# Optimization experiments

Measured on AMD Instinct MI355X. Metric: run time of the kernel, lower is better.

## Reference

```python
import jax, jax.numpy as jnp
import numpy as np

HEAD_NUM = 8
NEG = 10000.0


def setup_inputs() -> dict:
    key = jax.random.key(0)
    ks = jax.random.split(key, 8)
    B, S, D = 2, 2048, 512
    sc = 1.0 / np.sqrt(D)
    return {
        "x": jax.random.normal(ks[0], (B, S, D), dtype=jnp.float32),
        "mask": jax.random.randint(ks[1], (B, S), 0, 2, dtype=jnp.int32),
        "Wq": jax.random.normal(ks[2], (D, D), dtype=jnp.float32) * sc,
        "bq": jnp.zeros((D,), jnp.float32),
        "Wk": jax.random.normal(ks[3], (D, D), dtype=jnp.float32) * sc,
        "bk": jnp.zeros((D,), jnp.float32),
        "Wv": jax.random.normal(ks[4], (D, D), dtype=jnp.float32) * sc,
        "bv": jnp.zeros((D,), jnp.float32),
        "Wo": jax.random.normal(ks[5], (D, D), dtype=jnp.float32) * sc,
        "bo": jnp.zeros((D,), jnp.float32),
    }


def _split_heads(t, H):
    B, S, D = t.shape
    return t.reshape(B, S, H, D // H).transpose(0, 2, 1, 3)  # [B,H,S,hd]


def reference(x, mask, Wq, bq, Wk, bk, Wv, bv, Wo, bo):
    B, S, D = x.shape
    H = HEAD_NUM
    hd = D // H
    # linear projections + relu activation (as in keras layer)
    q = jax.nn.relu(x @ Wq + bq)
    k = jax.nn.relu(x @ Wk + bk)
    v = jax.nn.relu(x @ Wv + bv)
    q = _split_heads(q, H)
    k = _split_heads(k, H)
    v = _split_heads(v, H)
    # scaled dot-product scores: scale by sqrt(head_dim) (query last dim after split)
    e = jnp.einsum("bhqd,bhkd->bhqk", q, k) / jnp.sqrt(jnp.float32(hd))
    # causal (history_only) additive mask
    idx = jnp.arange(S)
    causal = (idx[None, :] > idx[:, None]).astype(jnp.float32)  # [S,S]
    e = e - NEG * causal[None, None, :, :]
    # key padding mask, additive
    e = e - NEG * (1.0 - mask.astype(jnp.float32))[:, None, None, :]
    # stable softmax (explicit max-subtract as in source)
    a = jax.nn.softmax(e, axis=-1)
    out = jnp.einsum("bhqk,bhkd->bhqd", a, v)  # [B,H,S,hd]
    out = out.transpose(0, 2, 1, 3).reshape(B, S, D)
    # output projection + activation
    return jax.nn.relu(out @ Wo + bo)
```

## Files before the change

### kernel.cpp

```cpp
#include <hip/hip_runtime.h>
#include <hip/hip_bf16.h>

constexpr int Bc = 2, Sc = 2048, Dc = 512, Hc = 8, HDc = 64;
constexpr int Mtot = Bc * Sc;
constexpr size_t HEADMAT = (size_t)Bc * Hc * Sc * HDc;
constexpr float SC2  = 0.18033688011112042f;
constexpr float NEG2 = 14426.950408889634f;

typedef __attribute__((ext_vector_type(8))) short          short8;
typedef __attribute__((ext_vector_type(8))) unsigned short ushort8;
typedef __attribute__((ext_vector_type(4))) float          f32x4;

#define MFMA16 __builtin_amdgcn_mfma_f32_16x16x32_bf16

static __device__ __forceinline__ unsigned short f32_to_bf16_bits(float f) {
    unsigned int u = __builtin_bit_cast(unsigned int, f);
    unsigned int r = u + 0x7FFFu + ((u >> 16) & 1u);
    return (unsigned short)(r >> 16);
}

__global__ __launch_bounds__(256)
void convert_x(const float* __restrict__ x, unsigned short* __restrict__ Xb, int n)
{
    const int i = (blockIdx.x * 256 + threadIdx.x) * 4;
    if (i >= n) return;
    const float4 v = *(const float4*)(x + i);
    ushort4 o;
    o.x = f32_to_bf16_bits(v.x);
    o.y = f32_to_bf16_bits(v.y);
    o.z = f32_to_bf16_bits(v.z);
    o.w = f32_to_bf16_bits(v.w);
    *(ushort4*)(Xb + i) = o;
}

__global__ __launch_bounds__(256)
void transpose_w(const float* __restrict__ W0, const float* __restrict__ W1,
                 const float* __restrict__ W2, const float* __restrict__ W3,
                 unsigned short* __restrict__ Wt)
{
    __shared__ float T[64][65];
    const int z = blockIdx.z;
    const float* Wp = (z == 0) ? W0 : (z == 1) ? W1 : (z == 2) ? W2 : W3;
    unsigned short* Op = Wt + (size_t)z * 512 * 512;

    const int kt = blockIdx.y * 64, nt = blockIdx.x * 64;
    const int t = threadIdx.x;
    const int r  = t >> 2, c4 = (t & 3) * 16;

    #pragma unroll
    for (int i = 0; i < 4; ++i) {
        const float4 v = *(const float4*)(Wp + (size_t)(kt + r) * 512 + nt + c4 + 4 * i);
        T[r][c4 + 4*i + 0] = v.x;
        T[r][c4 + 4*i + 1] = v.y;
        T[r][c4 + 4*i + 2] = v.z;
        T[r][c4 + 4*i + 3] = v.w;
    }
    __syncthreads();

    const int n = t >> 2, k4 = (t & 3) * 16;
    #pragma unroll
    for (int i = 0; i < 4; ++i) {
        ushort4 o;
        o.x = f32_to_bf16_bits(T[k4 + 4*i + 0][n]);
        o.y = f32_to_bf16_bits(T[k4 + 4*i + 1][n]);
        o.z = f32_to_bf16_bits(T[k4 + 4*i + 2][n]);
        o.w = f32_to_bf16_bits(T[k4 + 4*i + 3][n]);
        *(ushort4*)(Op + (size_t)(nt + n) * 512 + kt + k4 + 4 * i) = o;
    }
}

template<bool HEADOUT>
__global__ __launch_bounds__(256)
void gemm_tile(const unsigned short* __restrict__ Xb,
               const unsigned short* __restrict__ Wt,
               const float* __restrict__ b0, const float* __restrict__ b1,
               const float* __restrict__ b2,
               unsigned short* __restrict__ Hout,
               float* __restrict__ Yf)
{
    __shared__ short As[128 * 32];
    __shared__ short Bs[64 * 32];

    const int lane = threadIdx.x & 63, wave = threadIdx.x >> 6;
    const int c = lane & 15, g = lane >> 4;
    const int wr = wave >> 1, wc = wave & 1;
    const int z = blockIdx.z;
    const unsigned short* Wp = Wt + (size_t)z * 512 * 512;
    const float* bp = (z == 0) ? b0 : (z == 1) ? b1 : b2;
    const int bm = blockIdx.y * 128;
    const int bn = blockIdx.x * 64;

    const int srow = lane >> 2;
    const int scol = (lane & 3) * 8;

    f32x4 acc[4][2] = {};

    for (int k0 = 0; k0 < 512; k0 += 32) {
        __syncthreads();
        #pragma unroll
        for (int i = 0; i < 2; ++i) {
            const int row = (wave * 2 + i) * 16 + srow;
            const short8 v = *(const short8*)(Xb + (size_t)(bm + row) * 512 + k0 + scol);
            *(short8*)(&As[row * 32 + scol]) = v;
        }
        {
            const int row = wave * 16 + srow;
            const short8 v = *(const short8*)(Wp + (size_t)(bn + row) * 512 + k0 + scol);
            *(short8*)(&Bs[row * 32 + scol]) = v;
        }
        __syncthreads();

        short8 a[4], bfr[2];
        #pragma unroll
        for (int mi = 0; mi < 4; ++mi)
            a[mi] = *(const short8*)(&As[(wr * 64 + mi * 16 + c) * 32 + g * 8]);
        #pragma unroll
        for (int ni = 0; ni < 2; ++ni)
            bfr[ni] = *(const short8*)(&Bs[(wc * 32 + ni * 16 + c) * 32 + g * 8]);
        #pragma unroll
        for (int mi = 0; mi < 4; ++mi)
            #pragma unroll
            for (int ni = 0; ni < 2; ++ni)
                acc[mi][ni] = MFMA16(a[mi], bfr[ni], acc[mi][ni], 0, 0, 0);
    }

    #pragma unroll
    for (int mi = 0; mi < 4; ++mi) {
        #pragma unroll
        for (int ni = 0; ni < 2; ++ni) {
            const int n = bn + wc * 32 + ni * 16 + c;
            const float bias = bp[n];
            float v[4];
            #pragma unroll
            for (int r = 0; r < 4; ++r)
                v[r] = fmaxf(acc[mi][ni][r] + bias, 0.0f);
            const int mbase = bm + wr * 64 + mi * 16 + 4 * g;
            if constexpr (HEADOUT) {
                const int bb = mbase >> 11, ss = mbase & 2047;
                const int hh = n >> 6, hd = n & 63;
                #pragma unroll
                for (int r = 0; r < 4; ++r)
                    Hout[(size_t)z * HEADMAT +
                         (((size_t)(bb * Hc + hh) * Sc + ss + r) * HDc + hd)] =
                        f32_to_bf16_bits(v[r]);
            } else {
                #pragma unroll
                for (int r = 0; r < 4; ++r)
                    Yf[(size_t)(mbase + r) * 512 + n] = v[r];
            }
        }
    }
}

__global__ __launch_bounds__(256)
void attn_mfma(const short* __restrict__ Qh, const short* __restrict__ Kh,
               const short* __restrict__ Vh, const int* __restrict__ mask,
               unsigned short* __restrict__ Ob)
{
    __shared__ __align__(16) char smem[4 * 9216];

    const int lane = threadIdx.x & 63;
    const int wave = threadIdx.x >> 6;
    const int bid  = blockIdx.x;
    const int swz  = (bid & 7) * 128 + (bid >> 3);
    const int qt   = swz & 63;
    const int h    = (swz >> 6) & 7;
    const int b    = swz >> 9;
    const int q0   = qt * 32;
    const int c    = lane & 15;
    const int g    = lane >> 4;

    char*  wbase = smem + wave * 9216;
    short* vst   = (short*)wbase;
    float* Lacc  = (float*)wbase;
    float* Lml   = (float*)(wbase + 8704);

    const size_t headoff = (size_t)(b * Hc + h) * Sc * HDc;
    const short* Qp = Qh + headoff;
    const short* Kp = Kh + headoff;
    const short* Vp = Vh + headoff;
    const int* mb = mask + b * Sc;

    int fb = Sc;
    for (int base = 0; base < Sc; base += 64) {
        unsigned long long bal = __ballot(mb[base + lane] != 0);
        if (bal) { fb = base + (__ffsll(bal) - 1); break; }
    }
    const int kmax = (fb <= q0) ? (q0 + 32) : Sc;
    const int kend = (kmax + 31) & ~31;
    const int nT   = kend >> 5;
    const int tpw  = (nT + 3) >> 2;
    const int kbeg = wave * tpw * 32;
    const int kfin = min(kend, kbeg + tpw * 32);

    const short8 qa0 = *(const short8*)(Qp + (size_t)(q0 + c) * HDc + g * 8);
    const short8 qa1 = *(const short8*)(Qp + (size_t)(q0 + c) * HDc + 32 + g * 8);
    const short8 qb0 = *(const short8*)(Qp + (size_t)(q0 + 16 + c) * HDc + g * 8);
    const short8 qb1 = *(const short8*)(Qp + (size_t)(q0 + 16 + c) * HDc + 32 + g * 8);

    f32x4 accA[4] = {{0,0,0,0},{0,0,0,0},{0,0,0,0},{0,0,0,0}};
    f32x4 accB[4] = {{0,0,0,0},{0,0,0,0},{0,0,0,0},{0,0,0,0}};
    float mA = -1e30f, lA = 0.f, mB = -1e30f, lB = 0.f;

    const int vrow = lane >> 1;
    const int vcol = (lane & 1) * 32;

    for (int k0 = kbeg; k0 < kfin; k0 += 32) {
        const short* vsrc = Vp + (size_t)(k0 + vrow) * HDc + vcol;
        const ushort8 vr0 = *(const ushort8*)(vsrc + 0);
        const ushort8 vr1 = *(const ushort8*)(vsrc + 8);
        const ushort8 vr2 = *(const ushort8*)(vsrc + 16);
        const ushort8 vr3 = *(const ushort8*)(vsrc + 24);

        const short8 kf0a = *(const short8*)(Kp + (size_t)(k0 + c) * HDc + g * 8);
        const short8 kf0b = *(const short8*)(Kp + (size_t)(k0 + c) * HDc + 32 + g * 8);
        const short8 kf1a = *(const short8*)(Kp + (size_t)(k0 + 16 + c) * HDc + g * 8);
        const short8 kf1b = *(const short8*)(Kp + (size_t)(k0 + 16 + c) * HDc + 32 + g * 8);

        f32x4 sa0 = {0,0,0,0}, sa1 = {0,0,0,0};
        f32x4 sb0 = {0,0,0,0}, sb1 = {0,0,0,0};
        sa0 = MFMA16(kf0a, qa0, sa0, 0, 0, 0);
        sa0 = MFMA16(kf0b, qa1, sa0, 0, 0, 0);
        sa1 = MFMA16(kf1a, qa0, sa1, 0, 0, 0);
        sa1 = MFMA16(kf1b, qa1, sa1, 0, 0, 0);
        sb0 = MFMA16(kf0a, qb0, sb0, 0, 0, 0);
        sb0 = MFMA16(kf0b, qb1, sb0, 0, 0, 0);
        sb1 = MFMA16(kf1a, qb0, sb1, 0, 0, 0);
        sb1 = MFMA16(kf1b, qb1, sb1, 0, 0, 0);

        const int4 mka = *(const int4*)(mb + k0 + 4 * g);
        const int4 mkb = *(const int4*)(mb + k0 + 16 + 4 * g);
        const int mia[4] = {mka.x, mka.y, mka.z, mka.w};
        const int mib[4] = {mkb.x, mkb.y, mkb.z, mkb.w};

        float eA[8], eB[8];
        float tA = -1e30f, tB = -1e30f;
        if (k0 + 31 > q0) {
            #pragma unroll
            for (int r = 0; r < 4; ++r) {
                const int ka = k0 + 4 * g + r;
                const int kb = k0 + 16 + 4 * g + r;
                float e0 = sa0[r] * SC2; if (ka > q0 + c)      e0 -= NEG2;
                float e1 = sa1[r] * SC2; if (kb > q0 + c)      e1 -= NEG2;
                float e2 = sb0[r] * SC2; if (ka > q0 + 16 + c) e2 -= NEG2;
                float e3 = sb1[r] * SC2; if (kb > q0 + 16 + c) e3 -= NEG2;
                if (mia[r] == 0) { e0 -= NEG2; e2 -= NEG2; }
                if (mib[r] == 0) { e1 -= NEG2; e3 -= NEG2; }
                eA[r] = e0; eA[4 + r] = e1; tA = fmaxf(tA, fmaxf(e0, e1));
                eB[r] = e2; eB[4 + r] = e3; tB = fmaxf(tB, fmaxf(e2, e3));
            }
        } else {
            #pragma unroll
            for (int r = 0; r < 4; ++r) {
                float e0 = sa0[r] * SC2;
                float e1 = sa1[r] * SC2;
                float e2 = sb0[r] * SC2;
                float e3 = sb1[r] * SC2;
                if (mia[r] == 0) { e0 -= NEG2; e2 -= NEG2; }
                if (mib[r] == 0) { e1 -= NEG2; e3 -= NEG2; }
                eA[r] = e0; eA[4 + r] = e1; tA = fmaxf(tA, fmaxf(e0, e1));
                eB[r] = e2; eB[4 + r] = e3; tB = fmaxf(tB, fmaxf(e2, e3));
            }
        }
        tA = fmaxf(tA, __shfl_xor(tA, 16));
        tB = fmaxf(tB, __shfl_xor(tB, 16));
        tA = fmaxf(tA, __shfl_xor(tA, 32));
        tB = fmaxf(tB, __shfl_xor(tB, 32));

        if (__any(tA > mA)) {
            const float mn = fmaxf(mA, tA);
            const float corr = __builtin_exp2f(mA - mn);
            mA = mn; lA *= corr;
            float cq[4];
            #pragma unroll
            for (int r = 0; r < 4; ++r) cq[r] = __shfl(corr, 4 * g + r);
            #pragma unroll
            for (int t = 0; t < 4; ++t)
                #pragma unroll
                for (int r = 0; r < 4; ++r) accA[t][r] *= cq[r];
        }
        if (__any(tB > mB)) {
            const float mn = fmaxf(mB, tB);
            const float corr = __builtin_exp2f(mB - mn);
            mB = mn; lB *= corr;
            float cq[4];
            #pragma unroll
            for (int r = 0; r < 4; ++r) cq[r] = __shfl(corr, 4 * g + r);
            #pragma unroll
            for (int t = 0; t < 4; ++t)
                #pragma unroll
                for (int r = 0; r < 4; ++r) accB[t][r] *= cq[r];
        }

        float pA[8], pB[8], psA = 0.f, psB = 0.f;
        #pragma unroll
        for (int j = 0; j < 8; ++j) {
            pA[j] = __builtin_exp2f(eA[j] - mA); psA += pA[j];
            pB[j] = __builtin_exp2f(eB[j] - mB); psB += pB[j];
        }
        lA += psA; lB += psB;

        short8 pfa, pfb;
        #pragma unroll
        for (int j = 0; j < 8; ++j) {
            pfa[j] = (short)f32_to_bf16_bits(pA[j]);
            pfb[j] = (short)f32_to_bf16_bits(pB[j]);
        }

        short* vdst = vst + vrow * 72 + vcol;
        *(ushort8*)(vdst + 0)  = vr0;
        *(ushort8*)(vdst + 8)  = vr1;
        *(ushort8*)(vdst + 16) = vr2;
        *(ushort8*)(vdst + 24) = vr3;

        #pragma unroll
        for (int t = 0; t < 4; ++t) {
            short8 vf;
            #pragma unroll
            for (int j = 0; j < 4; ++j) {
                vf[j]     = vst[(4 * g + j) * 72      + t * 16 + c];
                vf[4 + j] = vst[(16 + 4 * g + j) * 72 + t * 16 + c];
            }
            accA[t] = MFMA16(pfa, vf, accA[t], 0, 0, 0);
            accB[t] = MFMA16(pfb, vf, accB[t], 0, 0, 0);
        }
    }

    lA += __shfl_xor(lA, 16); lA += __shfl_xor(lA, 32);
    lB += __shfl_xor(lB, 16); lB += __shfl_xor(lB, 32);

    if (g == 0) {
        Lml[c]      = mA;  Lml[16 + c] = mB;
        Lml[32 + c] = lA;  Lml[48 + c] = lB;
    }
    #pragma unroll
    for (int t = 0; t < 4; ++t)
        #pragma unroll
        for (int r = 0; r < 4; ++r) {
            Lacc[(4 * g + r) * 68 + t * 16 + c]      = accA[t][r];
            Lacc[(16 + 4 * g + r) * 68 + t * 16 + c] = accB[t][r];
        }
    __syncthreads();

    const int col = wave * 16 + c;
    #pragma unroll
    for (int half = 0; half < 2; ++half)
        #pragma unroll
        for (int r = 0; r < 4; ++r) {
            const int row = half * 16 + 4 * g + r;
            float mu[4], lu[4], ou[4], M = -1e30f;
            #pragma unroll
            for (int u = 0; u < 4; ++u) {
                const float* LaccU = (const float*)(smem + u * 9216);
                const float* LmlU  = (const float*)(smem + u * 9216 + 8704);
                mu[u] = LmlU[row];
                lu[u] = LmlU[32 + row];
                ou[u] = LaccU[row * 68 + col];
                M = fmaxf(M, mu[u]);
            }
            float L = 0.f, o = 0.f;
            #pragma unroll
            for (int u = 0; u < 4; ++u) {
                const float w = __builtin_exp2f(mu[u] - M);
                L += w * lu[u];
                o += w * ou[u];
            }
            Ob[(size_t)(b * Sc + q0 + row) * Dc + h * HDc + col] =
                f32_to_bf16_bits(o / L);
        }
}

extern "C" void kernel_launch(void* const* d_in, const int* in_sizes, int n_in,
                              void* d_out, int out_size, void* d_ws, size_t ws_size,
                              hipStream_t stream) {
    const float* x  = (const float*)d_in[0];
    const int* mask = (const int*)d_in[1];
    const float* Wq = (const float*)d_in[2];
    const float* bq = (const float*)d_in[3];
    const float* Wk = (const float*)d_in[4];
    const float* bk = (const float*)d_in[5];
    const float* Wv = (const float*)d_in[6];
    const float* bv = (const float*)d_in[7];
    const float* Wo = (const float*)d_in[8];
    const float* bo = (const float*)d_in[9];
    float* out = (float*)d_out;

    unsigned short* Xb = (unsigned short*)d_ws;
    unsigned short* Wt = Xb + (size_t)Mtot * 512;
    unsigned short* Qh = Wt + (size_t)4 * 512 * 512;
    unsigned short* Kh = Qh + HEADMAT;
    unsigned short* Vh = Kh + HEADMAT;
    unsigned short* Ob = Vh + HEADMAT;

    convert_x<<<dim3((Mtot * 512) / 1024), dim3(256), 0, stream>>>(
        x, Xb, Mtot * 512);
    transpose_w<<<dim3(8, 8, 4), dim3(256), 0, stream>>>(Wq, Wk, Wv, Wo, Wt);
    gemm_tile<true><<<dim3(8, Mtot / 128, 3), dim3(256), 0, stream>>>(
        Xb, Wt, bq, bk, bv, Qh, nullptr);
    attn_mfma<<<dim3(1024), dim3(256), 0, stream>>>(
        (const short*)Qh, (const short*)Kh, (const short*)Vh, mask, Ob);
    gemm_tile<false><<<dim3(8, Mtot / 128, 1), dim3(256), 0, stream>>>(
        Ob, Wt + (size_t)3 * 512 * 512, bo, bo, bo, nullptr, out);
}
```

Before: 109.7 us.

## Pair early and late 16-row query tiles per block to balance causal work

Each block now handles two 16-row query tiles, one near the start and one near the end of the sequence (p and 127-p), instead of one contiguous 32-row tile. When causal truncation applies, this balances per-block key-loop work across the grid. In exchange the K and V tiles are no longer shared between the two query halves, so each block loads K/V twice over its key ranges and issues half as many MFMAs per K load.

```diff
diff --git a/kernel.cpp b/kernel.cpp
--- a/kernel.cpp
+++ b/kernel.cpp
@@ -163,10 +163,11 @@
     const int wave = threadIdx.x >> 6;
     const int bid  = blockIdx.x;
     const int swz  = (bid & 7) * 128 + (bid >> 3);
-    const int qt   = swz & 63;
+    const int p    = swz & 63;
     const int h    = (swz >> 6) & 7;
     const int b    = swz >> 9;
-    const int q0   = qt * 32;
+    const int q0A  = p * 16;
+    const int q0B  = (127 - p) * 16;
     const int c    = lane & 15;
     const int g    = lane >> 4;
 
@@ -186,145 +187,118 @@
         unsigned long long bal = __ballot(mb[base + lane] != 0);
         if (bal) { fb = base + (__ffsll(bal) - 1); break; }
     }
-    const int kmax = (fb <= q0) ? (q0 + 32) : Sc;
-    const int kend = (kmax + 31) & ~31;
-    const int nT   = kend >> 5;
-    const int tpw  = (nT + 3) >> 2;
-    const int kbeg = wave * tpw * 32;
-    const int kfin = min(kend, kbeg + tpw * 32);
-
-    const short8 qa0 = *(const short8*)(Qp + (size_t)(q0 + c) * HDc + g * 8);
-    const short8 qa1 = *(const short8*)(Qp + (size_t)(q0 + c) * HDc + 32 + g * 8);
-    const short8 qb0 = *(const short8*)(Qp + (size_t)(q0 + 16 + c) * HDc + g * 8);
-    const short8 qb1 = *(const short8*)(Qp + (size_t)(q0 + 16 + c) * HDc + 32 + g * 8);
+
+    const int vrow = lane >> 1;
+    const int vcol = (lane & 1) * 32;
 
     f32x4 accA[4] = {{0,0,0,0},{0,0,0,0},{0,0,0,0},{0,0,0,0}};
     f32x4 accB[4] = {{0,0,0,0},{0,0,0,0},{0,0,0,0},{0,0,0,0}};
     float mA = -1e30f, lA = 0.f, mB = -1e30f, lB = 0.f;
 
-    const int vrow = lane >> 1;
-    const int vcol = (lane & 1) * 32;
-
-    for (int k0 = kbeg; k0 < kfin; k0 += 32) {
-        const short* vsrc = Vp + (size_t)(k0 + vrow) * HDc + vcol;
-        const ushort8 vr0 = *(const ushort8*)(vsrc + 0);
-        const ushort8 vr1 = *(const ushort8*)(vsrc + 8);
-        const ushort8 vr2 = *(const ushort8*)(vsrc + 16);
-        const ushort8 vr3 = *(const ushort8*)(vsrc + 24);
-
-        const short8 kf0a = *(const short8*)(Kp + (size_t)(k0 + c) * HDc + g * 8);
-        const short8 kf0b = *(const short8*)(Kp + (size_t)(k0 + c) * HDc + 32 + g * 8);
-        const short8 kf1a = *(const short8*)(Kp + (size_t)(k0 + 16 + c) * HDc + g * 8);
-        const short8 kf1b = *(const short8*)(Kp + (size_t)(k0 + 16 + c) * HDc + 32 + g * 8);
-
-        f32x4 sa0 = {0,0,0,0}, sa1 = {0,0,0,0};
-        f32x4 sb0 = {0,0,0,0}, sb1 = {0,0,0,0};
-        sa0 = MFMA16(kf0a, qa0, sa0, 0, 0, 0);
-        sa0 = MFMA16(kf0b, qa1, sa0, 0, 0, 0);
-        sa1 = MFMA16(kf1a, qa0, sa1, 0, 0, 0);
-        sa1 = MFMA16(kf1b, qa1, sa1, 0, 0, 0);
-        sb0 = MFMA16(kf0a, qb0, sb0, 0, 0, 0);
-        sb0 = MFMA16(kf0b, qb1, sb0, 0, 0, 0);
-        sb1 = MFMA16(kf1a, qb0, sb1, 0, 0, 0);
-        sb1 = MFMA16(kf1b, qb1, sb1, 0, 0, 0);
-
-        const int4 mka = *(const int4*)(mb + k0 + 4 * g);
-        const int4 mkb = *(const int4*)(mb + k0 + 16 + 4 * g);
-        const int mia[4] = {mka.x, mka.y, mka.z, mka.w};
-        const int mib[4] = {mkb.x, mkb.y, mkb.z, mkb.w};
-
-        float eA[8], eB[8];
-        float tA = -1e30f, tB = -1e30f;
-        if (k0 + 31 > q0) {
-            #pragma unroll
-            for (int r = 0; r < 4; ++r) {
-                const int ka = k0 + 4 * g + r;
-                const int kb = k0 + 16 + 4 * g + r;
-                float e0 = sa0[r] * SC2; if (ka > q0 + c)      e0 -= NEG2;
-                float e1 = sa1[r] * SC2; if (kb > q0 + c)      e1 -= NEG2;
-                float e2 = sb0[r] * SC2; if (ka > q0 + 16 + c) e2 -= NEG2;
-                float e3 = sb1[r] * SC2; if (kb > q0 + 16 + c) e3 -= NEG2;
-                if (mia[r] == 0) { e0 -= NEG2; e2 -= NEG2; }
-                if (mib[r] == 0) { e1 -= NEG2; e3 -= NEG2; }
-                eA[r] = e0; eA[4 + r] = e1; tA = fmaxf(tA, fmaxf(e0, e1));
-                eB[r] = e2; eB[4 + r] = e3; tB = fmaxf(tB, fmaxf(e2, e3));
-            }
-        } else {
-            #pragma unroll
-            for (int r = 0; r < 4; ++r) {
-                float e0 = sa0[r] * SC2;
-                float e1 = sa1[r] * SC2;
-                float e2 = sb0[r] * SC2;
-                float e3 = sb1[r] * SC2;
-                if (mia[r] == 0) { e0 -= NEG2; e2 -= NEG2; }
-                if (mib[r] == 0) { e1 -= NEG2; e3 -= NEG2; }
-                eA[r] = e0; eA[4 + r] = e1; tA = fmaxf(tA, fmaxf(e0, e1));
-                eB[r] = e2; eB[4 + r] = e3; tB = fmaxf(tB, fmaxf(e2, e3));
-            }
-        }
-        tA = fmaxf(tA, __shfl_xor(tA, 16));
-        tB = fmaxf(tB, __shfl_xor(tB, 16));
-        tA = fmaxf(tA, __shfl_xor(tA, 32));
-        tB = fmaxf(tB, __shfl_xor(tB, 32));
-
-        if (__any(tA > mA)) {
-            const float mn = fmaxf(mA, tA);
-            const float corr = __builtin_exp2f(mA - mn);
-            mA = mn; lA *= corr;
-            float cq[4];
-            #pragma unroll
-            for (int r = 0; r < 4; ++r) cq[r] = __shfl(corr, 4 * g + r);
-            #pragma unroll
-            for (int t = 0; t < 4; ++t)
-                #pragma unroll
-                for (int r = 0; r < 4; ++r) accA[t][r] *= cq[r];
-        }
-        if (__any(tB > mB)) {
-            const float mn = fmaxf(mB, tB);
-            const float corr = __builtin_exp2f(mB - mn);
-            mB = mn; lB *= corr;
-            float cq[4];
-            #pragma unroll
-            for (int r = 0; r < 4; ++r) cq[r] = __shfl(corr, 4 * g + r);
-            #pragma unroll
-            for (int t = 0; t < 4; ++t)
-                #pragma unroll
-                for (int r = 0; r < 4; ++r) accB[t][r] *= cq[r];
-        }
-
-        float pA[8], pB[8], psA = 0.f, psB = 0.f;
-        #pragma unroll
-        for (int j = 0; j < 8; ++j) {
-            pA[j] = __builtin_exp2f(eA[j] - mA); psA += pA[j];
-            pB[j] = __builtin_exp2f(eB[j] - mB); psB += pB[j];
-        }
-        lA += psA; lB += psB;
-
-        short8 pfa, pfb;
-        #pragma unroll
-        for (int j = 0; j < 8; ++j) {
-            pfa[j] = (short)f32_to_bf16_bits(pA[j]);
-            pfb[j] = (short)f32_to_bf16_bits(pB[j]);
-        }
-
-        short* vdst = vst + vrow * 72 + vcol;
-        *(ushort8*)(vdst + 0)  = vr0;
-        *(ushort8*)(vdst + 8)  = vr1;
-        *(ushort8*)(vdst + 16) = vr2;
-        *(ushort8*)(vdst + 24) = vr3;
-
-        #pragma unroll
-        for (int t = 0; t < 4; ++t) {
-            short8 vf;
-            #pragma unroll
-            for (int j = 0; j < 4; ++j) {
-                vf[j]     = vst[(4 * g + j) * 72      + t * 16 + c];
-                vf[4 + j] = vst[(16 + 4 * g + j) * 72 + t * 16 + c];
-            }
-            accA[t] = MFMA16(pfa, vf, accA[t], 0, 0, 0);
-            accB[t] = MFMA16(pfb, vf, accB[t], 0, 0, 0);
-        }
-    }
+#define TILE_LOOP(q0X, accX, mX, lX, qx0, qx1)                                 \
+    {                                                                          \
+        const int kmax = (fb <= (q0X)) ? ((q0X) + 16) : Sc;                    \
+        const int kend = (kmax + 31) & ~31;                                    \
+        const int nT   = kend >> 5;                                            \
+        const int tpw  = (nT + 3) >> 2;                                        \
+        const int kbeg = wave * tpw * 32;                                      \
+        const int kfin = min(kend, kbeg + tpw * 32);                           \
+        for (int k0 = kbeg; k0 < kfin; k0 += 32) {                             \
+            const short* vsrc = Vp + (size_t)(k0 + vrow) * HDc + vcol;         \
+            const ushort8 vr0 = *(const ushort8*)(vsrc + 0);                   \
+            const ushort8 vr1 = *(const ushort8*)(vsrc + 8);                   \
+            const ushort8 vr2 = *(const ushort8*)(vsrc + 16);                  \
+            const ushort8 vr3 = *(const ushort8*)(vsrc + 24);                  \
+            const short8 kf0a = *(const short8*)(Kp + (size_t)(k0 + c) * HDc + g * 8);        \
+            const short8 kf0b = *(const short8*)(Kp + (size_t)(k0 + c) * HDc + 32 + g * 8);   \
+            const short8 kf1a = *(const short8*)(Kp + (size_t)(k0 + 16 + c) * HDc + g * 8);   \
+            const short8 kf1b = *(const short8*)(Kp + (size_t)(k0 + 16 + c) * HDc + 32 + g * 8);\
+            f32x4 s0 = {0,0,0,0}, s1 = {0,0,0,0};                              \
+            s0 = MFMA16(kf0a, qx0, s0, 0, 0, 0);                               \
+            s0 = MFMA16(kf0b, qx1, s0, 0, 0, 0);                               \
+            s1 = MFMA16(kf1a, qx0, s1, 0, 0, 0);                               \
+            s1 = MFMA16(kf1b, qx1, s1, 0, 0, 0);                               \
+            const int4 mka = *(const int4*)(mb + k0 + 4 * g);                  \
+            const int4 mkb = *(const int4*)(mb + k0 + 16 + 4 * g);             \
+            const int mia[4] = {mka.x, mka.y, mka.z, mka.w};                   \
+            const int mib[4] = {mkb.x, mkb.y, mkb.z, mkb.w};                   \
+            float e[8];                                                        \
+            float tmax = -1e30f;                                               \
+            if (k0 + 31 > (q0X)) {                                             \
+                _Pragma("unroll")                                              \
+                for (int r = 0; r < 4; ++r) {                                  \
+                    const int ka = k0 + 4 * g + r;                             \
+                    const int kb2 = k0 + 16 + 4 * g + r;                       \
+                    float e0 = s0[r] * SC2; if (ka  > (q0X) + c) e0 -= NEG2;   \
+                    float e1 = s1[r] * SC2; if (kb2 > (q0X) + c) e1 -= NEG2;   \
+                    if (mia[r] == 0) e0 -= NEG2;                               \
+                    if (mib[r] == 0) e1 -= NEG2;                               \
+                    e[r] = e0; e[4 + r] = e1;                                  \
+                    tmax = fmaxf(tmax, fmaxf(e0, e1));                         \
+                }                                                              \
+            } else {                                                           \
+                _Pragma("unroll")                                              \
+                for (int r = 0; r < 4; ++r) {                                  \
+                    float e0 = s0[r] * SC2;                                    \
+                    float e1 = s1[r] * SC2;                                    \
+                    if (mia[r] == 0) e0 -= NEG2;                               \
+                    if (mib[r] == 0) e1 -= NEG2;                               \
+                    e[r] = e0; e[4 + r] = e1;                                  \
+                    tmax = fmaxf(tmax, fmaxf(e0, e1));                         \
+                }                                                              \
+            }                                                                  \
+            tmax = fmaxf(tmax, __shfl_xor(tmax, 16));                          \
+            tmax = fmaxf(tmax, __shfl_xor(tmax, 32));                          \
+            if (__any(tmax > (mX))) {                                          \
+                const float mn = fmaxf((mX), tmax);                            \
+                const float corr = __builtin_exp2f((mX) - mn);                 \
+                (mX) = mn; (lX) *= corr;                                       \
+                float cq[4];                                                   \
+                _Pragma("unroll")                                              \
+                for (int r = 0; r < 4; ++r) cq[r] = __shfl(corr, 4 * g + r);   \
+                _Pragma("unroll")                                              \
+                for (int t = 0; t < 4; ++t)                                    \
+                    _Pragma("unroll")                                          \
+                    for (int r = 0; r < 4; ++r) (accX)[t][r] *= cq[r];         \
+            }                                                                  \
+            float pv[8], ps = 0.f;                                             \
+            _Pragma("unroll")                                                  \
+            for (int j = 0; j < 8; ++j) {                                      \
+                pv[j] = __builtin_exp2f(e[j] - (mX)); ps += pv[j];             \
+            }                                                                  \
+            (lX) += ps;                                                        \
+            short8 pf;                                                         \
+            _Pragma("unroll")                                                  \
+            for (int j = 0; j < 8; ++j) pf[j] = (short)f32_to_bf16_bits(pv[j]);\
+            short* vdst = vst + vrow * 72 + vcol;                              \
+            *(ushort8*)(vdst + 0)  = vr0;                                      \
+            *(ushort8*)(vdst + 8)  = vr1;                                      \
+            *(ushort8*)(vdst + 16) = vr2;                                      \
+            *(ushort8*)(vdst + 24) = vr3;                                      \
+            _Pragma("unroll")                                                  \
+            for (int t = 0; t < 4; ++t) {                                      \
+                short8 vf;                                                     \
+                _Pragma("unroll")                                              \
+                for (int j = 0; j < 4; ++j) {                                  \
+                    vf[j]     = vst[(4 * g + j) * 72      + t * 16 + c];       \
+                    vf[4 + j] = vst[(16 + 4 * g + j) * 72 + t * 16 + c];       \
+                }                                                              \
+                (accX)[t] = MFMA16(pf, vf, (accX)[t], 0, 0, 0);                \
+            }                                                                  \
+        }                                                                      \
+    }
+
+    {
+        const short8 qa0 = *(const short8*)(Qp + (size_t)(q0A + c) * HDc + g * 8);
+        const short8 qa1 = *(const short8*)(Qp + (size_t)(q0A + c) * HDc + 32 + g * 8);
+        TILE_LOOP(q0A, accA, mA, lA, qa0, qa1)
+    }
+    {
+        const short8 qb0 = *(const short8*)(Qp + (size_t)(q0B + c) * HDc + g * 8);
+        const short8 qb1 = *(const short8*)(Qp + (size_t)(q0B + c) * HDc + 32 + g * 8);
+        TILE_LOOP(q0B, accB, mB, lB, qb0, qb1)
+    }
+#undef TILE_LOOP
 
     lA += __shfl_xor(lA, 16); lA += __shfl_xor(lA, 32);
     lB += __shfl_xor(lB, 16); lB += __shfl_xor(lB, 32);
@@ -348,13 +322,14 @@
         #pragma unroll
         for (int r = 0; r < 4; ++r) {
             const int row = half * 16 + 4 * g + r;
+            const int qout = (half ? q0B : q0A) + 4 * g + r;
             float mu[4], lu[4], ou[4], M = -1e30f;
             #pragma unroll
             for (int u = 0; u < 4; ++u) {
                 const float* LaccU = (const float*)(smem + u * 9216);
                 const float* LmlU  = (const float*)(smem + u * 9216 + 8704);
-                mu[u] = LmlU[row];
-                lu[u] = LmlU[32 + row];
+                mu[u] = LmlU[half * 16 + ((row) & 15)];
+                lu[u] = LmlU[32 + half * 16 + ((row) & 15)];
                 ou[u] = LaccU[row * 68 + col];
                 M = fmaxf(M, mu[u]);
             }
@@ -365,7 +340,7 @@
                 L += w * lu[u];
                 o += w * ou[u];
             }
-            Ob[(size_t)(b * Sc + q0 + row) * Dc + h * HDc + col] =
+            Ob[(size_t)(b * Sc + qout) * Dc + h * HDc + col] =
                 f32_to_bf16_bits(o / L);
         }
 }
```

After: 107.4 us. -2.1%, faster.
